# Kernel optimization log

Hardware: AMD Instinct MI355X
Metric: run time of the kernel (lower is better)

Reference implementation:

```python
import jax, jax.numpy as jnp
import numpy as np

NUM_GROUPS = 32
EPS = 1e-5


def group_norm(x, weight, bias):
    # x: (B, C, H, W, D); normalize per (group, spatial) per sample
    b, c, h, w, d = x.shape
    g = NUM_GROUPS
    xg = x.reshape(b, g, c // g, h, w, d)
    mean = xg.mean(axis=(2, 3, 4, 5), keepdims=True)
    var = xg.var(axis=(2, 3, 4, 5), keepdims=True)
    xg = (xg - mean) * jax.lax.rsqrt(var + EPS)
    xn = xg.reshape(b, c, h, w, d)
    return xn * weight[None, :, None, None, None] + bias[None, :, None, None, None]


def setup_inputs() -> dict:
    key = jax.random.key(0)
    ks = jax.random.split(key, 7)
    B, C, H, W, D = 4, 128, 16, 16, 16
    x = jax.random.normal(ks[0], (B, C, H, W, D), dtype=jnp.float32)
    gn_w = jnp.ones((C,), dtype=jnp.float32)
    gn_b = jnp.zeros((C,), dtype=jnp.float32)
    s = 1.0 / np.sqrt(C)
    qkv_w = jax.random.uniform(ks[1], (3 * C, C), minval=-s, maxval=s, dtype=jnp.float32)
    qkv_b = jax.random.uniform(ks[2], (3 * C,), minval=-s, maxval=s, dtype=jnp.float32)
    out_w = jax.random.uniform(ks[3], (C, C), minval=-s, maxval=s, dtype=jnp.float32)
    out_b = jax.random.uniform(ks[4], (C,), minval=-s, maxval=s, dtype=jnp.float32)
    return {"x": x, "gn_w": gn_w, "gn_b": gn_b, "qkv_w": qkv_w,
            "qkv_b": qkv_b, "out_w": out_w, "out_b": out_b}


def reference(x, gn_w, gn_b, qkv_w, qkv_b, out_w, out_b):
    b, c, h, w, d = x.shape
    n = h * w * d
    xn = group_norm(x, gn_w, gn_b)
    # 1x1x1 conv == pointwise linear over channels
    qkv = jnp.einsum('bchwd,oc->bohwd', xn, qkv_w) + qkv_b[None, :, None, None, None]
    q, k, v = jnp.split(qkv, 3, axis=1)
    q = q.transpose(0, 2, 3, 4, 1).reshape(b, n, c)   # (b, n, c)
    k = k.reshape(b, c, n)                             # (b, c, n)
    v = v.transpose(0, 2, 3, 4, 1).reshape(b, n, c)   # (b, n, c)
    scores = jnp.einsum('bnc,bcm->bnm', q, k) * (c ** -0.5)
    attn = jax.nn.softmax(scores, axis=-1)
    out = jnp.einsum('bnm,bmc->bnc', attn, v)          # (b, n, c)
    out = out.reshape(b, h, w, d, c).transpose(0, 4, 1, 2, 3)
    out = jnp.einsum('bchwd,oc->bohwd', out, out_w) + out_b[None, :, None, None, None]
    return out + x
```

## Files before the change

### kernel.cpp

```cpp
#include <hip/hip_runtime.h>

typedef unsigned short u16;
typedef __attribute__((ext_vector_type(8))) short bf16x8;
typedef __attribute__((ext_vector_type(4))) float f32x4;

__device__ __forceinline__ u16 f2bf(float f) {
    union { float f; unsigned u; } v; v.f = f;
    unsigned r = v.u + 0x7fffu + ((v.u >> 16) & 1u);
    return (u16)(r >> 16);
}

__device__ __forceinline__ void gload16(const u16* g, char* l) {
    __builtin_amdgcn_global_load_lds(
        (const __attribute__((address_space(1))) unsigned int*)g,
        (__attribute__((address_space(3))) unsigned int*)l, 16, 0, 0);
}

__global__ __launch_bounds__(256)
void k_stats(const float* __restrict__ x, float* __restrict__ mean, float* __restrict__ rstd)
{
    int bg = blockIdx.x, t = threadIdx.x;
    const float4* xp = (const float4*)(x + (size_t)bg * 16384);
    float s1 = 0.f, s2 = 0.f;
#pragma unroll
    for (int i = 0; i < 16; ++i) {
        float4 v = xp[i * 256 + t];
        s1 += v.x + v.y + v.z + v.w;
        s2 += v.x * v.x + v.y * v.y + v.z * v.z + v.w * v.w;
    }
#pragma unroll
    for (int off = 32; off >= 1; off >>= 1) {
        s1 += __shfl_xor(s1, off);
        s2 += __shfl_xor(s2, off);
    }
    __shared__ float a1[4], a2[4];
    if ((t & 63) == 0) { a1[t >> 6] = s1; a2[t >> 6] = s2; }
    __syncthreads();
    if (t == 0) {
        float t1 = a1[0] + a1[1] + a1[2] + a1[3];
        float t2 = a2[0] + a2[1] + a2[2] + a2[3];
        float mu = t1 * (1.f / 16384.f);
        float var = t2 * (1.f / 16384.f) - mu * mu;
        mean[bg] = mu;
        rstd[bg] = rsqrtf(var + 1e-5f);
    }
}

__global__ __launch_bounds__(384)
void k_qkv(const float* __restrict__ x, const float* __restrict__ gn_w, const float* __restrict__ gn_b,
           const float* __restrict__ qkv_w, const float* __restrict__ qkv_b,
           const float* __restrict__ mean, const float* __restrict__ rstd,
           u16* __restrict__ Qo, u16* __restrict__ Ko, u16* __restrict__ Vo)
{
    __shared__ float xn[128][64];
    int t = threadIdx.x;
    int b = blockIdx.x >> 6;
    int n0 = (blockIdx.x & 63) << 6;

    for (int e = t; e < 8192; e += 384) {
        int c = e >> 6, nn = e & 63;
        int bg = (b << 5) + (c >> 2);
        float sc = rstd[bg] * gn_w[c];
        float sh = gn_b[c] - mean[bg] * sc;
        xn[c][nn] = x[(size_t)(b * 128 + c) * 4096 + n0 + nn] * sc + sh;
    }
    __syncthreads();

    const int og = t >> 2;
    const int ng = t & 3;

    float acc[4][16];
#pragma unroll
    for (int i = 0; i < 4; ++i) {
        float bs = qkv_b[og * 4 + i];
#pragma unroll
        for (int j = 0; j < 16; ++j) acc[i][j] = bs;
    }

    const float4* wr0 = (const float4*)(qkv_w + (size_t)(og * 4 + 0) * 128);
    const float4* wr1 = (const float4*)(qkv_w + (size_t)(og * 4 + 1) * 128);
    const float4* wr2 = (const float4*)(qkv_w + (size_t)(og * 4 + 2) * 128);
    const float4* wr3 = (const float4*)(qkv_w + (size_t)(og * 4 + 3) * 128);

    for (int c4 = 0; c4 < 32; ++c4) {
        float4 w0 = wr0[c4], w1 = wr1[c4], w2 = wr2[c4], w3 = wr3[c4];
#pragma unroll
        for (int cc = 0; cc < 4; ++cc) {
            int c = c4 * 4 + cc;
            float v0 = (cc == 0) ? w0.x : (cc == 1) ? w0.y : (cc == 2) ? w0.z : w0.w;
            float v1 = (cc == 0) ? w1.x : (cc == 1) ? w1.y : (cc == 2) ? w1.z : w1.w;
            float v2 = (cc == 0) ? w2.x : (cc == 1) ? w2.y : (cc == 2) ? w2.z : w2.w;
            float v3 = (cc == 0) ? w3.x : (cc == 1) ? w3.y : (cc == 2) ? w3.z : w3.w;
#pragma unroll
            for (int j4 = 0; j4 < 4; ++j4) {
                float4 xv = *(const float4*)&xn[c][ng * 16 + j4 * 4];
#pragma unroll
                for (int jj = 0; jj < 4; ++jj) {
                    float xs = (jj == 0) ? xv.x : (jj == 1) ? xv.y : (jj == 2) ? xv.z : xv.w;
                    acc[0][j4 * 4 + jj] = fmaf(xs, v0, acc[0][j4 * 4 + jj]);
                    acc[1][j4 * 4 + jj] = fmaf(xs, v1, acc[1][j4 * 4 + jj]);
                    acc[2][j4 * 4 + jj] = fmaf(xs, v2, acc[2][j4 * 4 + jj]);
                    acc[3][j4 * 4 + jj] = fmaf(xs, v3, acc[3][j4 * 4 + jj]);
                }
            }
        }
    }

    const float qscale = 0.08838834764831845f * 1.4426950408889634f;
    if (og < 32) {
        size_t base = (size_t)(b * 4096 + n0 + ng * 16) * 128 + og * 4;
#pragma unroll
        for (int n = 0; n < 16; ++n) {
            uint2 pk;
            pk.x = ((unsigned)f2bf(acc[1][n] * qscale) << 16) | f2bf(acc[0][n] * qscale);
            pk.y = ((unsigned)f2bf(acc[3][n] * qscale) << 16) | f2bf(acc[2][n] * qscale);
            *(uint2*)&Qo[base + (size_t)n * 128] = pk;
        }
    } else if (og < 64) {
        size_t base = (size_t)(b * 4096 + n0 + ng * 16) * 128 + (og - 32) * 4;
#pragma unroll
        for (int n = 0; n < 16; ++n) {
            uint2 pk;
            pk.x = ((unsigned)f2bf(acc[1][n]) << 16) | f2bf(acc[0][n]);
            pk.y = ((unsigned)f2bf(acc[3][n]) << 16) | f2bf(acc[2][n]);
            *(uint2*)&Ko[base + (size_t)n * 128] = pk;
        }
    } else {
#pragma unroll
        for (int i = 0; i < 4; ++i) {
            size_t base = (size_t)(b * 128 + (og - 64) * 4 + i) * 4096 + n0 + ng * 16;
            uint4 pa, pb;
            pa.x = ((unsigned)f2bf(acc[i][1]) << 16) | f2bf(acc[i][0]);
            pa.y = ((unsigned)f2bf(acc[i][3]) << 16) | f2bf(acc[i][2]);
            pa.z = ((unsigned)f2bf(acc[i][5]) << 16) | f2bf(acc[i][4]);
            pa.w = ((unsigned)f2bf(acc[i][7]) << 16) | f2bf(acc[i][6]);
            pb.x = ((unsigned)f2bf(acc[i][9]) << 16) | f2bf(acc[i][8]);
            pb.y = ((unsigned)f2bf(acc[i][11]) << 16) | f2bf(acc[i][10]);
            pb.z = ((unsigned)f2bf(acc[i][13]) << 16) | f2bf(acc[i][12]);
            pb.w = ((unsigned)f2bf(acc[i][15]) << 16) | f2bf(acc[i][14]);
            *(uint4*)&Vo[base] = pa;
            *(uint4*)&Vo[base + 8] = pb;
        }
    }
}

__global__ __launch_bounds__(256, 2)
void k_attn(const u16* __restrict__ Qg, const u16* __restrict__ Kg, const u16* __restrict__ Vg,
            float* __restrict__ Opart, float* __restrict__ ml,
            int split, int kvlen, int iters)
{
    __shared__ __align__(16) u16 Kl[2][64 * 128];
    __shared__ __align__(16) u16 Vl[2][128 * 64];
    __shared__ __align__(16) u16 Pl[4 * 32 * 64];

    const int t = threadIdx.x;
    const int blk = blockIdx.x;
    int half, qt, b;
    if (split == 4) {
        int idx = blk >> 3;
        qt = idx & 31;
        int c = (blk & 7) + ((idx >> 5) << 3);
        b = c >> 2;
        half = c & 3;
    } else {
        half = blk % split;
        qt = (blk / split) & 31;
        b = blk / (split * 32);
    }
    const int w = t >> 6;
    const int lane = t & 63;
    const int l15 = lane & 15;
    const int l4 = lane >> 4;
    const int q0 = qt << 7;
    const int swz = (l15 & 7) << 4;

    bf16x8 qf[2][4];
#pragma unroll
    for (int qh = 0; qh < 2; ++qh) {
        const u16* qb = Qg + (size_t)(b * 4096 + q0 + w * 32 + qh * 16 + l15) * 128 + l4 * 8;
#pragma unroll
        for (int kc = 0; kc < 4; ++kc) qf[qh][kc] = *(const bf16x8*)(qb + kc * 32);
    }
    f32x4 oac[2][8];
#pragma unroll
    for (int qh = 0; qh < 2; ++qh)
#pragma unroll
        for (int cf = 0; cf < 8; ++cf) oac[qh][cf] = (f32x4){0.f, 0.f, 0.f, 0.f};
    float m[2] = {-__builtin_inff(), -__builtin_inff()};
    float lsum[2] = {0.f, 0.f};

    const int kv0 = half * kvlen;
    char* plw = (char*)Pl + w * 4096;

    const int krow = lane >> 4;
    const int vrow = lane >> 3;
    const int kcolA = ((lane & 15) ^ krow) * 8;
    const int kcolB = ((lane & 15) ^ (krow + 4)) * 8;
    const int vcol  = ((lane & 7) ^ (vrow & 7)) * 8;
    const u16* KgB = Kg + (size_t)b * 4096 * 128;
    const u16* VgB = Vg + (size_t)b * 128 * 4096;

    auto STAGE = [&](int buf, int kvb) {
        char* kd = (char*)&Kl[buf][0] + w * 4096;
        char* vd = (char*)&Vl[buf][0] + w * 4096;
        const u16* kga = KgB + (size_t)(kvb + 16 * w) * 128;
        const u16* vga = VgB + kvb + (size_t)(32 * w) * 4096;
#pragma unroll
        for (int i = 0; i < 4; ++i) {
            gload16(kga + (size_t)(4 * i + krow) * 128 + ((i & 1) ? kcolB : kcolA),
                    kd + i * 1024);
            gload16(vga + (size_t)(8 * i + vrow) * 4096 + vcol,
                    vd + i * 1024);
        }
    };

    STAGE(0, kv0);
    __syncthreads();

    int cur = 0;
    for (int it = 0; it < iters; ++it) {
        if (it + 1 < iters) STAGE(cur ^ 1, kv0 + (it + 1) * 64);

        const char* kb = (const char*)&Kl[cur][0];
        f32x4 st[2][4];
        __builtin_amdgcn_s_setprio(1);
#pragma unroll
        for (int mt = 0; mt < 4; ++mt) {
            f32x4 s0 = (f32x4){0.f, 0.f, 0.f, 0.f};
            f32x4 s1 = (f32x4){0.f, 0.f, 0.f, 0.f};
#pragma unroll
            for (int kc = 0; kc < 4; ++kc) {
                bf16x8 kf = *(const bf16x8*)(kb + (mt * 16 + l15) * 256 +
                                             ((kc * 64 + l4 * 16) ^ swz));
                s0 = __builtin_amdgcn_mfma_f32_16x16x32_bf16(kf, qf[0][kc], s0, 0, 0, 0);
                s1 = __builtin_amdgcn_mfma_f32_16x16x32_bf16(kf, qf[1][kc], s1, 0, 0, 0);
            }
            st[0][mt] = s0;
            st[1][mt] = s1;
        }
        __builtin_amdgcn_s_setprio(0);

#pragma unroll
        for (int qh = 0; qh < 2; ++qh) {
            float pmax = -__builtin_inff();
#pragma unroll
            for (int mt = 0; mt < 4; ++mt)
                pmax = fmaxf(pmax, fmaxf(fmaxf(st[qh][mt][0], st[qh][mt][1]),
                                         fmaxf(st[qh][mt][2], st[qh][mt][3])));
            pmax = fmaxf(pmax, __shfl_xor(pmax, 16));
            pmax = fmaxf(pmax, __shfl_xor(pmax, 32));

            if (!__all(pmax - m[qh] <= 8.f)) {
                float nm = fmaxf(m[qh], pmax);
                float fr = __builtin_amdgcn_exp2f(m[qh] - nm);
                m[qh] = nm;
                lsum[qh] *= fr;
#pragma unroll
                for (int cf = 0; cf < 8; ++cf)
#pragma unroll
                    for (int r = 0; r < 4; ++r) oac[qh][cf][r] *= fr;
            }

            float rsum = 0.f;
            uint2 pw[4];
#pragma unroll
            for (int mt = 0; mt < 4; ++mt) {
                float p0 = __builtin_amdgcn_exp2f(st[qh][mt][0] - m[qh]);
                float p1 = __builtin_amdgcn_exp2f(st[qh][mt][1] - m[qh]);
                float p2 = __builtin_amdgcn_exp2f(st[qh][mt][2] - m[qh]);
                float p3 = __builtin_amdgcn_exp2f(st[qh][mt][3] - m[qh]);
                rsum += (p0 + p1) + (p2 + p3);
                pw[mt].x = ((unsigned)f2bf(p1) << 16) | f2bf(p0);
                pw[mt].y = ((unsigned)f2bf(p3) << 16) | f2bf(p2);
            }
            rsum += __shfl_xor(rsum, 16);
            rsum += __shfl_xor(rsum, 32);
            lsum[qh] += rsum;

#pragma unroll
            for (int mt = 0; mt < 4; ++mt)
                *(uint2*)(plw + (qh * 16 + l15) * 128 + ((mt * 32 + l4 * 8) ^ swz)) = pw[mt];
        }
        asm volatile("s_waitcnt lgkmcnt(0)" ::: "memory");
        __builtin_amdgcn_sched_barrier(0);

        const char* vb = (const char*)&Vl[cur][0];
        __builtin_amdgcn_s_setprio(1);
#pragma unroll
        for (int kc2 = 0; kc2 < 2; ++kc2) {
            bf16x8 pf0 = *(const bf16x8*)(plw + (0 * 16 + l15) * 128 + ((kc2 * 64 + l4 * 16) ^ swz));
            bf16x8 pf1 = *(const bf16x8*)(plw + (1 * 16 + l15) * 128 + ((kc2 * 64 + l4 * 16) ^ swz));
#pragma unroll
            for (int cf = 0; cf < 8; ++cf) {
                bf16x8 vf = *(const bf16x8*)(vb + (cf * 16 + l15) * 128 +
                                             ((kc2 * 64 + l4 * 16) ^ swz));
                oac[0][cf] = __builtin_amdgcn_mfma_f32_16x16x32_bf16(vf, pf0, oac[0][cf], 0, 0, 0);
                oac[1][cf] = __builtin_amdgcn_mfma_f32_16x16x32_bf16(vf, pf1, oac[1][cf], 0, 0, 0);
            }
        }
        __builtin_amdgcn_s_setprio(0);
        __syncthreads();
        cur ^= 1;
    }

#pragma unroll
    for (int qh = 0; qh < 2; ++qh) {
        size_t qrow = ((size_t)half * 4 + b) * 4096 + q0 + w * 32 + qh * 16 + l15;
        float* orow = Opart + qrow * 128;
#pragma unroll
        for (int cf = 0; cf < 8; ++cf) {
            float4 v;
            v.x = oac[qh][cf][0]; v.y = oac[qh][cf][1];
            v.z = oac[qh][cf][2]; v.w = oac[qh][cf][3];
            *(float4*)&orow[cf * 16 + l4 * 4] = v;
        }
        if (l4 == 0) {
            size_t mb = (size_t)half * 16384 + b * 4096 + q0 + w * 32 + qh * 16 + l15;
            ml[mb * 2 + 0] = m[qh];
            ml[mb * 2 + 1] = lsum[qh];
        }
    }
}

__global__ __launch_bounds__(256)
void k_proj(const float* __restrict__ Opart, const float* __restrict__ ml,
            const float* __restrict__ x, const float* __restrict__ out_w,
            const float* __restrict__ out_b, float* __restrict__ out, int split)
{
    __shared__ float Ol[128][64];
    int t = threadIdx.x;
    int b = blockIdx.x >> 6;
    int n0 = (blockIdx.x & 63) << 6;

    for (int e = t; e < 2048; e += 256) {
        int nn = e >> 5, c4 = e & 31;
        size_t rg = (size_t)b * 4096 + n0 + nn;
        float msv[4], lsv[4];
#pragma unroll
        for (int s = 0; s < 4; ++s) {
            if (s < split) {
                msv[s] = ml[((size_t)s * 16384 + rg) * 2 + 0];
                lsv[s] = ml[((size_t)s * 16384 + rg) * 2 + 1];
            } else { msv[s] = -__builtin_inff(); lsv[s] = 0.f; }
        }
        float mm = fmaxf(fmaxf(msv[0], msv[1]), fmaxf(msv[2], msv[3]));
        float es[4]; float L = 0.f;
#pragma unroll
        for (int s = 0; s < 4; ++s) {
            es[s] = (s < split) ? __builtin_amdgcn_exp2f(msv[s] - mm) : 0.f;
            L += lsv[s] * es[s];
        }
        float inv = 1.f / L;
        float ox = 0.f, oy = 0.f, oz = 0.f, ow = 0.f;
#pragma unroll
        for (int s = 0; s < 4; ++s) {
            if (s < split) {
                float4 o4 = *(const float4*)&Opart[((size_t)s * 16384 + rg) * 128 + c4 * 4];
                ox = fmaf(o4.x, es[s], ox); oy = fmaf(o4.y, es[s], oy);
                oz = fmaf(o4.z, es[s], oz); ow = fmaf(o4.w, es[s], ow);
            }
        }
        Ol[c4 * 4 + 0][nn] = ox * inv;
        Ol[c4 * 4 + 1][nn] = oy * inv;
        Ol[c4 * 4 + 2][nn] = oz * inv;
        Ol[c4 * 4 + 3][nn] = ow * inv;
    }
    __syncthreads();

    const int ocg = t & 31;
    const int ng = t >> 5;

    float acc[4][8];
#pragma unroll
    for (int i = 0; i < 4; ++i) {
        float bs = out_b[ocg * 4 + i];
#pragma unroll
        for (int j = 0; j < 8; ++j) acc[i][j] = bs;
    }

    const float4* wr0 = (const float4*)(out_w + (size_t)(ocg * 4 + 0) * 128);
    const float4* wr1 = (const float4*)(out_w + (size_t)(ocg * 4 + 1) * 128);
    const float4* wr2 = (const float4*)(out_w + (size_t)(ocg * 4 + 2) * 128);
    const float4* wr3 = (const float4*)(out_w + (size_t)(ocg * 4 + 3) * 128);

    for (int c4 = 0; c4 < 32; ++c4) {
        float4 w0 = wr0[c4], w1 = wr1[c4], w2 = wr2[c4], w3 = wr3[c4];
#pragma unroll
        for (int cc = 0; cc < 4; ++cc) {
            int c = c4 * 4 + cc;
            float v0 = (cc == 0) ? w0.x : (cc == 1) ? w0.y : (cc == 2) ? w0.z : w0.w;
            float v1 = (cc == 0) ? w1.x : (cc == 1) ? w1.y : (cc == 2) ? w1.z : w1.w;
            float v2 = (cc == 0) ? w2.x : (cc == 1) ? w2.y : (cc == 2) ? w2.z : w2.w;
            float v3 = (cc == 0) ? w3.x : (cc == 1) ? w3.y : (cc == 2) ? w3.z : w3.w;
#pragma unroll
            for (int j4 = 0; j4 < 2; ++j4) {
                float4 xv = *(const float4*)&Ol[c][ng * 8 + j4 * 4];
#pragma unroll
                for (int jj = 0; jj < 4; ++jj) {
                    float xs = (jj == 0) ? xv.x : (jj == 1) ? xv.y : (jj == 2) ? xv.z : xv.w;
                    acc[0][j4 * 4 + jj] = fmaf(xs, v0, acc[0][j4 * 4 + jj]);
                    acc[1][j4 * 4 + jj] = fmaf(xs, v1, acc[1][j4 * 4 + jj]);
                    acc[2][j4 * 4 + jj] = fmaf(xs, v2, acc[2][j4 * 4 + jj]);
                    acc[3][j4 * 4 + jj] = fmaf(xs, v3, acc[3][j4 * 4 + jj]);
                }
            }
        }
    }

#pragma unroll
    for (int i = 0; i < 4; ++i) {
        size_t ob = (size_t)(b * 128 + ocg * 4 + i) * 4096 + n0 + ng * 8;
#pragma unroll
        for (int j4 = 0; j4 < 2; ++j4) {
            float4 xr = *(const float4*)&x[ob + j4 * 4];
            float4 ov;
            ov.x = acc[i][j4 * 4 + 0] + xr.x;
            ov.y = acc[i][j4 * 4 + 1] + xr.y;
            ov.z = acc[i][j4 * 4 + 2] + xr.z;
            ov.w = acc[i][j4 * 4 + 3] + xr.w;
            *(float4*)&out[ob + j4 * 4] = ov;
        }
    }
}

extern "C" void kernel_launch(void* const* d_in, const int* in_sizes, int n_in,
                              void* d_out, int out_size, void* d_ws, size_t ws_size,
                              hipStream_t stream)
{
    const float* x     = (const float*)d_in[0];
    const float* gn_w  = (const float*)d_in[1];
    const float* gn_b  = (const float*)d_in[2];
    const float* qkv_w = (const float*)d_in[3];
    const float* qkv_b = (const float*)d_in[4];
    const float* out_w = (const float*)d_in[5];
    const float* out_b = (const float*)d_in[6];
    float* out = (float*)d_out;

    char* ws = (char*)d_ws;
    float* mean  = (float*)ws;
    float* rstd  = (float*)(ws + 512);
    u16*   Q     = (u16*)(ws + 4096);
    u16*   K     = (u16*)(ws + 4198400);
    u16*   V     = (u16*)(ws + 8392704);
    float* mlb   = (float*)(ws + 12587008);
    float* Opart = (float*)(ws + 13111296);

    int split = (ws_size >= (size_t)46700000) ? 4 : 2;
    int kvlen = 4096 / split;
    int iters = kvlen / 64;

    k_stats<<<128, 256, 0, stream>>>(x, mean, rstd);
    k_qkv<<<256, 384, 0, stream>>>(x, gn_w, gn_b, qkv_w, qkv_b, mean, rstd, Q, K, V);
    k_attn<<<128 * split, 256, 0, stream>>>(Q, K, V, Opart, mlb, split, kvlen, iters);
    k_proj<<<256, 256, 0, stream>>>(Opart, mlb, x, out_w, out_b, out, split);
}
```

Baseline: 126.3 us.

## Load V fragments directly from global, store partial outputs as bf16, raise split

The attention kernel stops staging V through LDS and instead loads V fragments straight from global memory into registers each iteration. This halves LDS use so occupancy can rise to three blocks per CU. Partial outputs are converted to bf16 and written with coalesced stores through an LDS transpose, which halves Opart traffic. The KV split rises to 8 (or 4 as the fallback), adding more blocks and more combine work in the projection kernel. The risks are exposed global-load latency for V in the inner loop and lower precision in the partial outputs.

```diff
diff --git a/kernel.cpp b/kernel.cpp
--- a/kernel.cpp
+++ b/kernel.cpp
@@ -8,6 +8,9 @@
     union { float f; unsigned u; } v; v.f = f;
     unsigned r = v.u + 0x7fffu + ((v.u >> 16) & 1u);
     return (u16)(r >> 16);
+}
+__device__ __forceinline__ float bf2f(unsigned lo16) {
+    union { unsigned u; float f; } v; v.u = lo16 << 16; return v.f;
 }
 
 __device__ __forceinline__ void gload16(const u16* g, char* l) {
@@ -144,19 +147,25 @@
     }
 }
 
-__global__ __launch_bounds__(256, 2)
+__global__ __launch_bounds__(256, 3)
 void k_attn(const u16* __restrict__ Qg, const u16* __restrict__ Kg, const u16* __restrict__ Vg,
-            float* __restrict__ Opart, float* __restrict__ ml,
+            u16* __restrict__ Opart, float* __restrict__ ml,
             int split, int kvlen, int iters)
 {
     __shared__ __align__(16) u16 Kl[2][64 * 128];
-    __shared__ __align__(16) u16 Vl[2][128 * 64];
     __shared__ __align__(16) u16 Pl[4 * 32 * 64];
 
     const int t = threadIdx.x;
     const int blk = blockIdx.x;
     int half, qt, b;
-    if (split == 4) {
+    if (split == 8) {
+        int xcd = blk & 7;
+        int idx = blk >> 3;
+        qt = idx & 31;
+        int combo = xcd + ((idx >> 5) << 3);
+        b = combo >> 3;
+        half = combo & 7;
+    } else if (split == 4) {
         int idx = blk >> 3;
         qt = idx & 31;
         int c = (blk & 7) + ((idx >> 5) << 3);
@@ -193,25 +202,18 @@
     char* plw = (char*)Pl + w * 4096;
 
     const int krow = lane >> 4;
-    const int vrow = lane >> 3;
     const int kcolA = ((lane & 15) ^ krow) * 8;
     const int kcolB = ((lane & 15) ^ (krow + 4)) * 8;
-    const int vcol  = ((lane & 7) ^ (vrow & 7)) * 8;
     const u16* KgB = Kg + (size_t)b * 4096 * 128;
-    const u16* VgB = Vg + (size_t)b * 128 * 4096;
+    const u16* VgB = Vg + (size_t)b * 128 * 4096 + (size_t)l15 * 4096 + l4 * 8;
 
     auto STAGE = [&](int buf, int kvb) {
         char* kd = (char*)&Kl[buf][0] + w * 4096;
-        char* vd = (char*)&Vl[buf][0] + w * 4096;
         const u16* kga = KgB + (size_t)(kvb + 16 * w) * 128;
-        const u16* vga = VgB + kvb + (size_t)(32 * w) * 4096;
-#pragma unroll
-        for (int i = 0; i < 4; ++i) {
+#pragma unroll
+        for (int i = 0; i < 4; ++i)
             gload16(kga + (size_t)(4 * i + krow) * 128 + ((i & 1) ? kcolB : kcolA),
                     kd + i * 1024);
-            gload16(vga + (size_t)(8 * i + vrow) * 4096 + vcol,
-                    vd + i * 1024);
-        }
     };
 
     STAGE(0, kv0);
@@ -219,7 +221,13 @@
 
     int cur = 0;
     for (int it = 0; it < iters; ++it) {
-        if (it + 1 < iters) STAGE(cur ^ 1, kv0 + (it + 1) * 64);
+        int kvb = kv0 + it * 64;
+        if (it + 1 < iters) STAGE(cur ^ 1, kvb + 64);
+
+        bf16x8 vA[8];
+#pragma unroll
+        for (int cf = 0; cf < 8; ++cf)
+            vA[cf] = *(const bf16x8*)(VgB + (size_t)cf * 16 * 4096 + kvb);
 
         const char* kb = (const char*)&Kl[cur][0];
         f32x4 st[2][4];
@@ -284,46 +292,62 @@
         asm volatile("s_waitcnt lgkmcnt(0)" ::: "memory");
         __builtin_amdgcn_sched_barrier(0);
 
-        const char* vb = (const char*)&Vl[cur][0];
+        bf16x8 vB[8];
+#pragma unroll
+        for (int cf = 0; cf < 8; ++cf)
+            vB[cf] = *(const bf16x8*)(VgB + (size_t)cf * 16 * 4096 + kvb + 32);
+
+        bf16x8 pf0a = *(const bf16x8*)(plw + (0 * 16 + l15) * 128 + ((0 + l4 * 16) ^ swz));
+        bf16x8 pf1a = *(const bf16x8*)(plw + (1 * 16 + l15) * 128 + ((0 + l4 * 16) ^ swz));
+        bf16x8 pf0b = *(const bf16x8*)(plw + (0 * 16 + l15) * 128 + ((64 + l4 * 16) ^ swz));
+        bf16x8 pf1b = *(const bf16x8*)(plw + (1 * 16 + l15) * 128 + ((64 + l4 * 16) ^ swz));
         __builtin_amdgcn_s_setprio(1);
 #pragma unroll
-        for (int kc2 = 0; kc2 < 2; ++kc2) {
-            bf16x8 pf0 = *(const bf16x8*)(plw + (0 * 16 + l15) * 128 + ((kc2 * 64 + l4 * 16) ^ swz));
-            bf16x8 pf1 = *(const bf16x8*)(plw + (1 * 16 + l15) * 128 + ((kc2 * 64 + l4 * 16) ^ swz));
-#pragma unroll
-            for (int cf = 0; cf < 8; ++cf) {
-                bf16x8 vf = *(const bf16x8*)(vb + (cf * 16 + l15) * 128 +
-                                             ((kc2 * 64 + l4 * 16) ^ swz));
-                oac[0][cf] = __builtin_amdgcn_mfma_f32_16x16x32_bf16(vf, pf0, oac[0][cf], 0, 0, 0);
-                oac[1][cf] = __builtin_amdgcn_mfma_f32_16x16x32_bf16(vf, pf1, oac[1][cf], 0, 0, 0);
-            }
+        for (int cf = 0; cf < 8; ++cf) {
+            oac[0][cf] = __builtin_amdgcn_mfma_f32_16x16x32_bf16(vA[cf], pf0a, oac[0][cf], 0, 0, 0);
+            oac[1][cf] = __builtin_amdgcn_mfma_f32_16x16x32_bf16(vA[cf], pf1a, oac[1][cf], 0, 0, 0);
+        }
+#pragma unroll
+        for (int cf = 0; cf < 8; ++cf) {
+            oac[0][cf] = __builtin_amdgcn_mfma_f32_16x16x32_bf16(vB[cf], pf0b, oac[0][cf], 0, 0, 0);
+            oac[1][cf] = __builtin_amdgcn_mfma_f32_16x16x32_bf16(vB[cf], pf1b, oac[1][cf], 0, 0, 0);
         }
         __builtin_amdgcn_s_setprio(0);
         __syncthreads();
         cur ^= 1;
     }
 
-#pragma unroll
-    for (int qh = 0; qh < 2; ++qh) {
-        size_t qrow = ((size_t)half * 4 + b) * 4096 + q0 + w * 32 + qh * 16 + l15;
-        float* orow = Opart + qrow * 128;
-#pragma unroll
-        for (int cf = 0; cf < 8; ++cf) {
-            float4 v;
-            v.x = oac[qh][cf][0]; v.y = oac[qh][cf][1];
-            v.z = oac[qh][cf][2]; v.w = oac[qh][cf][3];
-            *(float4*)&orow[cf * 16 + l4 * 4] = v;
+    {
+        char* ow = (char*)&Kl[0][0] + w * 8192;
+#pragma unroll
+        for (int qh = 0; qh < 2; ++qh)
+#pragma unroll
+            for (int cf = 0; cf < 8; ++cf) {
+                uint2 pk;
+                pk.x = ((unsigned)f2bf(oac[qh][cf][1]) << 16) | f2bf(oac[qh][cf][0]);
+                pk.y = ((unsigned)f2bf(oac[qh][cf][3]) << 16) | f2bf(oac[qh][cf][2]);
+                *(uint2*)(ow + (qh * 16 + l15) * 256 + ((cf * 32 + l4 * 8) ^ ((l15 & 7) << 4))) = pk;
+            }
+        int r = lane >> 1, hb = lane & 1;
+        size_t qrow = ((size_t)half * 4 + b) * 4096 + q0 + w * 32 + r;
+        u16* orow = Opart + qrow * 128 + hb * 64;
+#pragma unroll
+        for (int i = 0; i < 8; ++i) {
+            uint4 d = *(uint4*)(ow + r * 256 + (((hb * 128) + i * 16) ^ ((r & 7) << 4)));
+            *(uint4*)(orow + i * 8) = d;
         }
         if (l4 == 0) {
-            size_t mb = (size_t)half * 16384 + b * 4096 + q0 + w * 32 + qh * 16 + l15;
-            ml[mb * 2 + 0] = m[qh];
-            ml[mb * 2 + 1] = lsum[qh];
+            size_t mb = (size_t)half * 16384 + b * 4096 + q0 + w * 32 + l15;
+            ml[mb * 2 + 0] = m[0];
+            ml[mb * 2 + 1] = lsum[0];
+            ml[(mb + 16) * 2 + 0] = m[1];
+            ml[(mb + 16) * 2 + 1] = lsum[1];
         }
     }
 }
 
 __global__ __launch_bounds__(256)
-void k_proj(const float* __restrict__ Opart, const float* __restrict__ ml,
+void k_proj(const u16* __restrict__ Opart, const float* __restrict__ ml,
             const float* __restrict__ x, const float* __restrict__ out_w,
             const float* __restrict__ out_b, float* __restrict__ out, int split)
 {
@@ -335,29 +359,32 @@
     for (int e = t; e < 2048; e += 256) {
         int nn = e >> 5, c4 = e & 31;
         size_t rg = (size_t)b * 4096 + n0 + nn;
-        float msv[4], lsv[4];
-#pragma unroll
-        for (int s = 0; s < 4; ++s) {
+        float mm = -__builtin_inff();
+        float msv[8], lsv[8];
+#pragma unroll
+        for (int s = 0; s < 8; ++s) {
             if (s < split) {
                 msv[s] = ml[((size_t)s * 16384 + rg) * 2 + 0];
                 lsv[s] = ml[((size_t)s * 16384 + rg) * 2 + 1];
+                mm = fmaxf(mm, msv[s]);
             } else { msv[s] = -__builtin_inff(); lsv[s] = 0.f; }
         }
-        float mm = fmaxf(fmaxf(msv[0], msv[1]), fmaxf(msv[2], msv[3]));
-        float es[4]; float L = 0.f;
-#pragma unroll
-        for (int s = 0; s < 4; ++s) {
+        float es[8]; float L = 0.f;
+#pragma unroll
+        for (int s = 0; s < 8; ++s) {
             es[s] = (s < split) ? __builtin_amdgcn_exp2f(msv[s] - mm) : 0.f;
             L += lsv[s] * es[s];
         }
         float inv = 1.f / L;
         float ox = 0.f, oy = 0.f, oz = 0.f, ow = 0.f;
 #pragma unroll
-        for (int s = 0; s < 4; ++s) {
+        for (int s = 0; s < 8; ++s) {
             if (s < split) {
-                float4 o4 = *(const float4*)&Opart[((size_t)s * 16384 + rg) * 128 + c4 * 4];
-                ox = fmaf(o4.x, es[s], ox); oy = fmaf(o4.y, es[s], oy);
-                oz = fmaf(o4.z, es[s], oz); ow = fmaf(o4.w, es[s], ow);
+                uint2 o2 = *(const uint2*)&Opart[((size_t)s * 16384 + rg) * 128 + c4 * 4];
+                ox = fmaf(bf2f(o2.x & 0xffffu), es[s], ox);
+                oy = fmaf(bf2f(o2.x >> 16), es[s], oy);
+                oz = fmaf(bf2f(o2.y & 0xffffu), es[s], oz);
+                ow = fmaf(bf2f(o2.y >> 16), es[s], ow);
             }
         }
         Ol[c4 * 4 + 0][nn] = ox * inv;
@@ -443,9 +470,9 @@
     u16*   K     = (u16*)(ws + 4198400);
     u16*   V     = (u16*)(ws + 8392704);
     float* mlb   = (float*)(ws + 12587008);
-    float* Opart = (float*)(ws + 13111296);
-
-    int split = (ws_size >= (size_t)46700000) ? 4 : 2;
+    u16*   Opart = (u16*)(ws + 13635584);
+
+    int split = (ws_size >= (size_t)47190016) ? 8 : 4;
     int kvlen = 4096 / split;
     int iters = kvlen / 64;
 
```

Result: slower. 247.3 us (+95.8%).
